# Kernel optimization log

Hardware: AMD Instinct MI355X
Metric: run time of the kernel (lower is better)

Reference implementation:

```python
import jax, jax.numpy as jnp
import numpy as np
import math

# ---- constants derived from PCF.__init__(nbbins=50, sigma=0.25, npoints=1024, n_rmax=5) ----
NBBINS = 50
SIGMA = 0.25
NPOINTS = 1024
N_RMAX = 5
RMAX = float(2.0 * np.sqrt(1.0 / (2.0 * np.sqrt(3.0) * NPOINTS)))
_STEP = N_RMAX / NBBINS
RS = np.array([(i + 1) * _STEP * RMAX for i in range(NBBINS)], dtype=np.float32)
AREA = np.array([math.pi * ((r + 0.5 * RMAX) ** 2 - max(0.0, r - 0.5 * RMAX) ** 2) for r in RS],
                dtype=np.float32)
GF = float(1.0 / (np.sqrt(math.pi) * SIGMA))


def _gaussian_kernel(x):
    return GF * jnp.exp(-(x * x) / (SIGMA * SIGMA))


def _perimeter_weight(x, y, rs):
    """x, y: [N] disk centers in [0,1]^2; rs: [B]. Returns [N, B] inverse in-domain perimeter fraction."""
    full = jnp.full((x.shape[0], rs.shape[0]), 2.0 * math.pi, dtype=x.dtype)

    def corr(full_angle, dx, dy):
        # dx, dy: [N] distance to a domain edge (as in the four blocks of perimeter_weight)
        mask = rs[None, :] > dx[:, None]                       # [N, B]
        alpha = jnp.arccos(jnp.clip(dx[:, None] / rs[None, :], -1.0, 1.0))
        sub = (jnp.minimum(alpha, jnp.arctan2(dy, dx)[:, None])
               + jnp.minimum(alpha, jnp.arctan2(1.0 - dy, dx)[:, None]))
        return full_angle - jnp.where(mask, sub, 0.0)

    full = corr(full, x, y)          # left edge
    full = corr(full, 1.0 - x, y)    # right edge
    full = corr(full, y, x)          # bottom edge
    full = corr(full, 1.0 - y, x)    # top edge
    peri = jnp.clip(full / (2.0 * math.pi), 0.0, 1.0)
    pos = peri > 0
    return jnp.where(pos, 1.0 / jnp.where(pos, peri, 1.0), 0.0)


def _disk_distance(pa, pb, rmax):
    """pa: [Na,3], pb: [Nb,3] disks (x, y, r) -> pairwise disk distance [Na, Nb] (repo utils.diskDistance)."""
    diff = pa[:, None, 0:2] - pb[None, :, 0:2]
    d = jnp.sqrt(jnp.sum(diff * diff, axis=-1))                # [Na, Nb]
    ra = pa[:, 2][:, None]
    rb = pb[None, :, 2]
    r1 = jnp.maximum(ra, rb)
    r2 = jnp.minimum(ra, rb)
    extent = jnp.maximum(d + r1 + r2, 2.0 * r1)
    overlap = jnp.clip(r1 + r2 - d, 0.0, None)
    return (extent - overlap + d + r1 - r2) / rmax


def _pcf_forward(disks_a, disks_b, same_category):
    rs = jnp.asarray(RS)
    area = jnp.asarray(AREA)
    na = disks_a.shape[0]
    nb = disks_b.shape[0]
    dist = _disk_distance(disks_a, disks_b, RMAX)              # [Na, Nb]
    # val[i, j, b] = gauss(rs_b / rmax - dist_ij)
    val = _gaussian_kernel(rs[None, None, :] / RMAX - dist[:, :, None])  # [Na, Nb, B]
    if same_category:
        # exclude self-pair j == i (torch.cat of slices around i)
        eye = jnp.eye(na, nb, dtype=val.dtype)
        val = val * (1.0 - eye)[:, :, None]
    contrib = jnp.sum(val, axis=1)                             # [Na, B]
    weights = _perimeter_weight(disks_a[:, 0], disks_a[:, 1], rs)  # [Na, B] (diskfact = 1/domainLength = 1)
    density = contrib * weights / area[None, :] / nb           # [Na, B]
    pcf_mean = jnp.sum(density, axis=0) / na                   # [B]
    pcf_lower = jnp.min(density, axis=0)
    pcf_upper = jnp.max(density, axis=0)
    pcf = jnp.stack([rs / RMAX, pcf_mean], axis=1)             # [B, 2]
    return pcf, pcf_lower, pcf_upper


def setup_inputs() -> dict:
    key = jax.random.key(0)
    ka, kb = jax.random.split(key)
    disks_a = jax.random.uniform(ka, (1024, 3), dtype=jnp.float32)
    disks_b = jax.random.uniform(kb, (1024, 3), dtype=jnp.float32)
    return {"disks_a": disks_a, "disks_b": disks_b, "same_category": 0}


def reference(disks_a, disks_b, same_category):
    return _pcf_forward(disks_a, disks_b, same_category)
```

## Files before the change

kernel.cpp:

```cpp
#include <hip/hip_runtime.h>
#include <math.h>

#define NB 50

__device__ __forceinline__ float dev_rmax() {
    return (float)(2.0 * sqrt(1.0 / (2.0 * sqrt(3.0) * 1024.0)));
}

__global__ void __launch_bounds__(256)
pcf_density_kernel(const float* __restrict__ da, const float* __restrict__ db,
                   const int* __restrict__ scp, float* __restrict__ dens,
                   int na, int nb)
{
    const float RMAX = dev_rmax();
    const float inv_rmax = 1.0f / RMAX;
    const float dd_cut = (3.75f * RMAX) * (3.75f * RMAX);
    const int i    = blockIdx.x;
    const int tid  = threadIdx.x;
    const int lane = tid & 63;
    const int wave = tid >> 6;
    const int sc   = scp[0];

    __shared__ float list[1024];
    __shared__ int   cnt;
    __shared__ float part[4 * NB];

    if (tid == 0) cnt = 0;

    const float ax = da[3*i+0];
    const float ay = da[3*i+1];
    const float ar = da[3*i+2];

    const float binf = 0.1f * (float)(lane + 1);
    float accb = 0.0f;

    __syncthreads();

    for (int base = 0; base < nb; base += 1024) {
        const int chunk = (nb - base < 1024) ? (nb - base) : 1024;
        if (chunk == 1024) {
            float bx[4], by[4], br[4];
#pragma unroll
            for (int k = 0; k < 4; ++k) {
                const int j = base + tid + 256 * k;
                bx[k] = db[3*j+0];
                by[k] = db[3*j+1];
                br[k] = db[3*j+2];
            }
#pragma unroll
            for (int k = 0; k < 4; ++k) {
                const int j = base + tid + 256 * k;
                const float dx = ax - bx[k];
                const float dy = ay - by[k];
                const float dd = dx*dx + dy*dy;
                if (dd < dd_cut && !((sc != 0) && (j == i))) {
                    const float d  = sqrtf(dd);
                    const float r1 = fmaxf(ar, br[k]);
                    const float r2 = fminf(ar, br[k]);
                    const float extent  = fmaxf(d + r1 + r2, 2.0f*r1);
                    const float overlap = fmaxf(r1 + r2 - d, 0.0f);
                    const float dist = (extent - overlap + d + r1 - r2) * inv_rmax;
                    if (dist < 7.5f) list[atomicAdd(&cnt, 1)] = dist;
                }
            }
        } else {
            for (int jo = tid; jo < chunk; jo += 256) {
                const int j = base + jo;
                const float bx = db[3*j+0];
                const float by = db[3*j+1];
                const float br = db[3*j+2];
                const float dx = ax - bx;
                const float dy = ay - by;
                const float dd = dx*dx + dy*dy;
                if (dd < dd_cut && !((sc != 0) && (j == i))) {
                    const float d  = sqrtf(dd);
                    const float r1 = fmaxf(ar, br);
                    const float r2 = fminf(ar, br);
                    const float extent  = fmaxf(d + r1 + r2, 2.0f*r1);
                    const float overlap = fmaxf(r1 + r2 - d, 0.0f);
                    const float dist = (extent - overlap + d + r1 - r2) * inv_rmax;
                    if (dist < 7.5f) list[atomicAdd(&cnt, 1)] = dist;
                }
            }
        }
        __syncthreads();

        const int M = cnt;
        for (int k = wave; k < M; k += 4) {
            const float x = binf - list[k];
            accb += __expf(-16.0f * x * x);
        }

        if (base + 1024 < nb) {
            __syncthreads();
            if (tid == 0) cnt = 0;
            __syncthreads();
        }
    }

    if (lane < NB) part[wave * NB + lane] = accb;
    __syncthreads();

    if (wave == 0 && lane < NB) {
        const float s = part[lane] + part[NB + lane] + part[2*NB + lane] + part[3*NB + lane];

        const float PI = 3.14159265358979323846f;
        const float GF = 1.0f / (sqrtf(PI) * 0.25f);
        const float rs = 0.1f * (float)(lane + 1) * RMAX;

        float full = 2.0f * PI;
        const float ex[4] = { ax, 1.0f - ax, ay, 1.0f - ay };
        const float ey[4] = { ay, ay,        ax, ax        };
#pragma unroll
        for (int c = 0; c < 4; ++c) {
            if (rs > ex[c]) {
                float ratio = ex[c] / rs;
                ratio = fminf(fmaxf(ratio, -1.0f), 1.0f);
                const float alpha = acosf(ratio);
                const float a1 = atan2f(ey[c], ex[c]);
                const float a2 = atan2f(1.0f - ey[c], ex[c]);
                full -= fminf(alpha, a1) + fminf(alpha, a2);
            }
        }
        float peri = full * (1.0f / (2.0f * PI));
        peri = fminf(fmaxf(peri, 0.0f), 1.0f);
        const float w = (peri > 0.0f) ? (1.0f / peri) : 0.0f;

        const float r_out = rs + 0.5f * RMAX;
        const float r_in  = fmaxf(rs - 0.5f * RMAX, 0.0f);
        const float area  = PI * (r_out * r_out - r_in * r_in);

        const float density = (GF * s) * w / area / (float)nb;
        dens[lane * na + i] = density;
    }
}

__global__ void __launch_bounds__(256)
pcf_reduce_kernel(const float* __restrict__ dens, float* __restrict__ out, int na)
{
    const int b    = blockIdx.x;
    const int tid  = threadIdx.x;
    const int lane = tid & 63;
    const int wave = tid >> 6;
    const float RMAX = dev_rmax();

    __shared__ float rs_[4], rmn[4], rmx[4];

    float s = 0.0f, mn = INFINITY, mx = -INFINITY;
    for (int i = tid; i < na; i += 256) {
        const float v = dens[b * na + i];
        s  += v;
        mn  = fminf(mn, v);
        mx  = fmaxf(mx, v);
    }
#pragma unroll
    for (int off = 32; off >= 1; off >>= 1) {
        s  += __shfl_down(s, off);
        mn  = fminf(mn, __shfl_down(mn, off));
        mx  = fmaxf(mx, __shfl_down(mx, off));
    }
    if (lane == 0) { rs_[wave] = s; rmn[wave] = mn; rmx[wave] = mx; }
    __syncthreads();
    if (tid == 0) {
        float ts = rs_[0] + rs_[1] + rs_[2] + rs_[3];
        float tmn = fminf(fminf(rmn[0], rmn[1]), fminf(rmn[2], rmn[3]));
        float tmx = fmaxf(fmaxf(rmx[0], rmx[1]), fmaxf(rmx[2], rmx[3]));
        const float rs = 0.1f * (float)(b + 1) * RMAX;
        out[2*b + 0] = rs / RMAX;
        out[2*b + 1] = ts / (float)na;
        out[100 + b] = tmn;
        out[150 + b] = tmx;
    }
}

extern "C" void kernel_launch(void* const* d_in, const int* in_sizes, int n_in,
                              void* d_out, int out_size, void* d_ws, size_t ws_size,
                              hipStream_t stream)
{
    const float* da = (const float*)d_in[0];
    const float* db = (const float*)d_in[1];
    const int*   sc = (const int*)d_in[2];
    float* out  = (float*)d_out;
    float* dens = (float*)d_ws;
    const int na = in_sizes[0] / 3;
    const int nb = in_sizes[1] / 3;

    pcf_density_kernel<<<na, 256, 0, stream>>>(da, db, sc, dens, na, nb);
    pcf_reduce_kernel<<<NB, 256, 0, stream>>>(dens, out, na);
}
```

Before: 63.35 us.

## Fuse density and reduction kernels with a global counter handoff

Merges the per-row density kernel and the per-bin reduction kernel into one launch. Extra trailing blocks spin on a global atomic counter until every density row has been published with atomics, then perform the min/max/mean reduction. The aim is to remove the second kernel launch and the gap between kernels. In exchange it adds a memset, atomic traffic and busy-waiting blocks, and it relies on the density blocks being scheduled before or alongside the waiting blocks to avoid deadlock.

```diff
diff --git a/kernel.cpp b/kernel.cpp
--- a/kernel.cpp
+++ b/kernel.cpp
@@ -7,19 +7,16 @@
     return (float)(2.0 * sqrt(1.0 / (2.0 * sqrt(3.0) * 1024.0)));
 }
 
-__global__ void __launch_bounds__(256)
-pcf_density_kernel(const float* __restrict__ da, const float* __restrict__ db,
-                   const int* __restrict__ scp, float* __restrict__ dens,
-                   int na, int nb)
+__device__ __forceinline__ float pcf_density_row(
+    const float* __restrict__ da, const float* __restrict__ db,
+    int sc, int i, int nb)
 {
     const float RMAX = dev_rmax();
     const float inv_rmax = 1.0f / RMAX;
     const float dd_cut = (3.75f * RMAX) * (3.75f * RMAX);
-    const int i    = blockIdx.x;
-    const int tid  = threadIdx.x;
-    const int lane = tid & 63;
-    const int wave = tid >> 6;
-    const int sc   = scp[0];
+    const int tid  = threadIdx.x;
+    const int lane = tid & 63;
+    const int wave = tid >> 6;
 
     __shared__ float list[1024];
     __shared__ int   cnt;
@@ -101,6 +98,7 @@
     if (lane < NB) part[wave * NB + lane] = accb;
     __syncthreads();
 
+    float density = 0.0f;
     if (wave == 0 && lane < NB) {
         const float s = part[lane] + part[NB + lane] + part[2*NB + lane] + part[3*NB + lane];
 
@@ -130,9 +128,23 @@
         const float r_in  = fmaxf(rs - 0.5f * RMAX, 0.0f);
         const float area  = PI * (r_out * r_out - r_in * r_in);
 
-        const float density = (GF * s) * w / area / (float)nb;
+        density = (GF * s) * w / area / (float)nb;
+    }
+    return density;
+}
+
+__global__ void __launch_bounds__(256)
+pcf_density_kernel(const float* __restrict__ da, const float* __restrict__ db,
+                   const int* __restrict__ scp, float* __restrict__ dens,
+                   int na, int nb)
+{
+    const int i    = blockIdx.x;
+    const int tid  = threadIdx.x;
+    const int lane = tid & 63;
+    const int wave = tid >> 6;
+    const float density = pcf_density_row(da, db, scp[0], i, nb);
+    if (wave == 0 && lane < NB)
         dens[lane * na + i] = density;
-    }
 }
 
 __global__ void __launch_bounds__(256)
@@ -173,6 +185,70 @@
     }
 }
 
+__global__ void __launch_bounds__(256)
+pcf_fused_kernel(const float* __restrict__ da, const float* __restrict__ db,
+                 const int* __restrict__ scp, unsigned* __restrict__ dens_bits,
+                 unsigned* __restrict__ counter, float* __restrict__ out,
+                 int na, int nb)
+{
+    const float RMAX = dev_rmax();
+    const int tid  = threadIdx.x;
+    const int lane = tid & 63;
+    const int wave = tid >> 6;
+
+    if ((int)blockIdx.x < na) {
+        const int i = blockIdx.x;
+        const float density = pcf_density_row(da, db, scp[0], i, nb);
+        if (wave == 0) {
+            if (lane < NB)
+                atomicExch(&dens_bits[lane * na + i], __float_as_uint(density));
+            asm volatile("s_waitcnt vmcnt(0)" ::: "memory");
+            if (tid == 0) atomicAdd(counter, 1u);
+        }
+    } else {
+        const int b = (int)blockIdx.x - na;
+
+        __shared__ int ready;
+        __shared__ float rs_[4], rmn[4], rmx[4];
+
+        if (tid == 0) ready = 0;
+        __syncthreads();
+        for (;;) {
+            if (tid == 0) ready = (atomicAdd(counter, 0u) >= (unsigned)na) ? 1 : 0;
+            __syncthreads();
+            if (ready) break;
+            __syncthreads();
+            __builtin_amdgcn_s_sleep(8);
+        }
+
+        float s = 0.0f, mn = INFINITY, mx = -INFINITY;
+        for (int i = tid; i < na; i += 256) {
+            const float v = __uint_as_float(atomicOr(&dens_bits[b * na + i], 0u));
+            s  += v;
+            mn  = fminf(mn, v);
+            mx  = fmaxf(mx, v);
+        }
+#pragma unroll
+        for (int off = 32; off >= 1; off >>= 1) {
+            s  += __shfl_down(s, off);
+            mn  = fminf(mn, __shfl_down(mn, off));
+            mx  = fmaxf(mx, __shfl_down(mx, off));
+        }
+        if (lane == 0) { rs_[wave] = s; rmn[wave] = mn; rmx[wave] = mx; }
+        __syncthreads();
+        if (tid == 0) {
+            float ts = rs_[0] + rs_[1] + rs_[2] + rs_[3];
+            float tmn = fminf(fminf(rmn[0], rmn[1]), fminf(rmn[2], rmn[3]));
+            float tmx = fmaxf(fmaxf(rmx[0], rmx[1]), fmaxf(rmx[2], rmx[3]));
+            const float rs = 0.1f * (float)(b + 1) * RMAX;
+            out[2*b + 0] = rs / RMAX;
+            out[2*b + 1] = ts / (float)na;
+            out[100 + b] = tmn;
+            out[150 + b] = tmx;
+        }
+    }
+}
+
 extern "C" void kernel_launch(void* const* d_in, const int* in_sizes, int n_in,
                               void* d_out, int out_size, void* d_ws, size_t ws_size,
                               hipStream_t stream)
@@ -181,10 +257,21 @@
     const float* db = (const float*)d_in[1];
     const int*   sc = (const int*)d_in[2];
     float* out  = (float*)d_out;
-    float* dens = (float*)d_ws;
     const int na = in_sizes[0] / 3;
     const int nb = in_sizes[1] / 3;
 
-    pcf_density_kernel<<<na, 256, 0, stream>>>(da, db, sc, dens, na, nb);
-    pcf_reduce_kernel<<<NB, 256, 0, stream>>>(dens, out, na);
-}
+    const size_t dens_bytes = (size_t)NB * (size_t)na * sizeof(float);
+    const size_t coff = (dens_bytes + 255) & ~(size_t)255;
+
+    if (ws_size >= coff + sizeof(unsigned)) {
+        unsigned* dens_bits = (unsigned*)d_ws;
+        unsigned* counter   = (unsigned*)((char*)d_ws + coff);
+        hipMemsetAsync(counter, 0, sizeof(unsigned), stream);
+        pcf_fused_kernel<<<na + NB, 256, 0, stream>>>(da, db, sc, dens_bits,
+                                                      counter, out, na, nb);
+    } else {
+        float* dens = (float*)d_ws;
+        pcf_density_kernel<<<na, 256, 0, stream>>>(da, db, sc, dens, na, nb);
+        pcf_reduce_kernel<<<NB, 256, 0, stream>>>(dens, out, na);
+    }
+}
```

New measurement: 80.77 us. +27.5%, slower.
